# Performance work log

Hardware: AMD Instinct MI355X
Metric: run time of the kernel (lower is better)

The kernel has to match this reference:

```python
import jax, jax.numpy as jnp
import numpy as np

N_NEURONS = 4096
N_EDGES = 131072
N_LAYERS = 2
VOCAB = 8192
B, T = 8, 128
DECAY = 0.99


def setup_inputs() -> dict:
    key = jax.random.key(0)
    ks = jax.random.split(key, 8)
    idx = jax.random.randint(ks[0], (B, T), 0, VOCAB)
    src = jax.random.randint(ks[1], (N_EDGES,), 0, N_NEURONS)
    dst = jax.random.randint(ks[2], (N_EDGES,), 0, N_NEURONS)
    Wemb = jax.random.normal(ks[3], (VOCAB, N_NEURONS), dtype=jnp.float32) * 0.02
    Gx = jax.random.normal(ks[4], (N_EDGES,), dtype=jnp.float32) * 0.02
    Gy = jax.random.normal(ks[5], (N_EDGES,), dtype=jnp.float32) * 0.02
    Gs = jnp.ones((N_EDGES,), dtype=jnp.float32)
    W_out = jax.random.normal(ks[6], (VOCAB, N_NEURONS), dtype=jnp.float32) * 0.02
    b_out = jnp.zeros((VOCAB,), dtype=jnp.float32)
    return {"idx": idx, "src": src, "dst": dst, "Wemb": Wemb, "Gx": Gx,
            "Gy": Gy, "Gs": Gs, "W_out": W_out, "b_out": b_out}


def reference(idx, src, dst, Wemb, Gx, Gy, Gs, W_out, b_out):
    # X: [B, T, n] token embeddings
    X = Wemb[idx]
    sigma0 = jnp.zeros((src.shape[0],), dtype=Wemb.dtype)
    y0 = X[:, 0, :]  # initial y_t = embedding of first token
    Xt = jnp.transpose(X, (1, 0, 2))  # [T, B, n] for scan over time

    def step(carry, x_t):
        y_t, sigma = carry
        for _ in range(N_LAYERS):
            # A[:, d] += x_t[:, s] * sigma  (gather-mul-scatter over edges)
            A = jnp.zeros_like(x_t).at[:, dst].add(x_t[:, src] * sigma)
            # Hebbian plasticity update on edge state sigma
            hebbian = (y_t[:, src] * x_t[:, dst]).mean(0)
            sigma = (sigma + hebbian * Gs) * DECAY
            y_t = jnp.zeros_like(x_t).at[:, dst].add(jax.nn.relu(A[:, src]) * Gy)
            x_t = jax.nn.relu(jnp.zeros_like(x_t).at[:, dst].add(y_t[:, src] * Gx))
        return (y_t, sigma), x_t

    (_, sigma_final), xs = jax.lax.scan(step, (y0, sigma0), Xt)  # xs: [T, B, n]
    logits = jnp.einsum('tbn,vn->btv', xs, W_out) + b_out  # [B, T, vocab]
    return logits, sigma_final
```

## Files before the change

### kernel.cpp

```cpp
#include <hip/hip_runtime.h>
#include <cstdint>
#include <cstddef>

#define NN   4096
#define NE   131072
#define NBAT 8
#define NT   128
#define NV   8192
#define NK   4096
#define NM   1024
#define DECAYF 0.99f
#define COOP_BLOCKS 256
#define COOP_THREADS 1024
#define NBARRIERS (NT * 5)

typedef short bf16x8 __attribute__((ext_vector_type(8)));
typedef float f32x4 __attribute__((ext_vector_type(4)));
typedef unsigned short u16x8 __attribute__((ext_vector_type(8)));

__device__ __forceinline__ unsigned short f2bf(float f) {
  unsigned int u = __builtin_bit_cast(unsigned int, f);
  u = u + 0x7fffu + ((u >> 16) & 1u);
  return (unsigned short)(u >> 16);
}

__device__ __forceinline__ float cload(const float* p) {
  return __hip_atomic_load(p, __ATOMIC_RELAXED, __HIP_MEMORY_SCOPE_AGENT);
}
__device__ __forceinline__ void cstore(float* p, float v) {
  __hip_atomic_store(p, v, __ATOMIC_RELAXED, __HIP_MEMORY_SCOPE_AGENT);
}
__device__ __forceinline__ int cloadi(const int* p) {
  return __hip_atomic_load(p, __ATOMIC_RELAXED, __HIP_MEMORY_SCOPE_AGENT);
}
__device__ __forceinline__ void cstorei(int* p, int v) {
  __hip_atomic_store(p, v, __ATOMIC_RELAXED, __HIP_MEMORY_SCOPE_AGENT);
}

__global__ void k_hist(const int* __restrict__ dst, int* __restrict__ cnt) {
  int e = blockIdx.x * 256 + threadIdx.x;
  if (e < NE) atomicAdd(&cnt[dst[e]], 1);
}

__global__ void k_scan(const int* __restrict__ cnt, int* __restrict__ row_ptr,
                       int* __restrict__ cursor) {
  __shared__ int lds[256];
  int tid = threadIdx.x;
  int base = tid * 16;
  int loc[16];
  int s = 0;
  #pragma unroll
  for (int i = 0; i < 16; ++i) { loc[i] = s; s += cnt[base + i]; }
  lds[tid] = s;
  __syncthreads();
  for (int off = 1; off < 256; off <<= 1) {
    int v = lds[tid];
    int a = (tid >= off) ? lds[tid - off] : 0;
    __syncthreads();
    lds[tid] = v + a;
    __syncthreads();
  }
  int myoff = (tid == 0) ? 0 : lds[tid - 1];
  #pragma unroll
  for (int i = 0; i < 16; ++i) {
    int rp = myoff + loc[i];
    row_ptr[base + i] = rp;
    cursor[base + i] = rp;
  }
  if (tid == 255) row_ptr[NN] = lds[255];
}

__global__ void k_build(const int* __restrict__ src, const int* __restrict__ dst,
                        const float* __restrict__ Gx, const float* __restrict__ Gy,
                        const float* __restrict__ Gs, int* __restrict__ cursor,
                        int* __restrict__ src_s, int* __restrict__ orig_s,
                        float* __restrict__ Gx_s, float* __restrict__ Gy_s,
                        float* __restrict__ Gs_s) {
  int e = blockIdx.x * 256 + threadIdx.x;
  if (e >= NE) return;
  int d = dst[e];
  int pos = atomicAdd(&cursor[d], 1);
  src_s[pos] = src[e];
  orig_s[pos] = e;
  Gx_s[pos] = Gx[e];
  Gy_s[pos] = Gy[e];
  Gs_s[pos] = Gs[e];
}

__global__ void k_gatherX(const int* __restrict__ idx, const float* __restrict__ Wemb,
                          float* __restrict__ Xbuf, float* __restrict__ ybuf) {
  __shared__ float tile[256 * 9];
  int t = blockIdx.x >> 4;
  int nc = (blockIdx.x & 15) << 8;
  int tid = threadIdx.x;
  #pragma unroll
  for (int bb = 0; bb < 8; ++bb) {
    int row = idx[bb * NT + t];
    tile[tid * 9 + bb] = Wemb[(size_t)row * NN + nc + tid];
  }
  __syncthreads();
  float* dp = Xbuf + (size_t)t * (NN * NBAT) + (size_t)nc * NBAT;
  #pragma unroll
  for (int kk = 0; kk < 8; ++kk) dp[tid * 8 + kk] = tile[tid * 9 + kk];
  if (t == 0) {
    float* yp = ybuf + (size_t)nc * NBAT;
    #pragma unroll
    for (int kk = 0; kk < 8; ++kk) yp[tid * 8 + kk] = tile[tid * 9 + kk];
  }
}

__global__ void k_convW(const float* __restrict__ W, unsigned short* __restrict__ Wbf) {
  size_t base = ((size_t)blockIdx.x * 256 + threadIdx.x) * 8;
  float4 a = *(const float4*)(W + base);
  float4 b = *(const float4*)(W + base + 4);
  u16x8 hv;
  hv[0] = f2bf(a.x); hv[1] = f2bf(a.y); hv[2] = f2bf(a.z); hv[3] = f2bf(a.w);
  hv[4] = f2bf(b.x); hv[5] = f2bf(b.y); hv[6] = f2bf(b.z); hv[7] = f2bf(b.w);
  *(u16x8*)(Wbf + base) = hv;
}

__device__ __forceinline__ void gridbar(int* bar, int& gen) {
  __syncthreads();
  if (threadIdx.x == 0) {
    cstorei(&bar[blockIdx.x], gen + 1);
    while (cloadi(&bar[320]) <= gen) __builtin_amdgcn_s_sleep(1);
  }
  ++gen;
  __syncthreads();
}

__global__ __launch_bounds__(COOP_THREADS, 8) void k_loop(
    const int* __restrict__ row_ptr, const int* __restrict__ src_s,
    const float* __restrict__ Gx_s, const float* __restrict__ Gy_s,
    const float* __restrict__ Gs_s, float* __restrict__ sigma_s,
    const float* __restrict__ Xbuf, float* __restrict__ ybuf,
    float* __restrict__ xbuf, float* __restrict__ Abuf,
    unsigned short* __restrict__ Abf, int* bar,
    const int* __restrict__ orig_s, float* __restrict__ sig_out) {
  if (blockIdx.x == COOP_BLOCKS) {
    if (threadIdx.x < 64) {
      const int lane = threadIdx.x;
      for (int g = 1; g <= NBARRIERS; ++g) {
        for (;;) {
          int v0 = cloadi(&bar[lane * 4 + 0]);
          int v1 = cloadi(&bar[lane * 4 + 1]);
          int v2 = cloadi(&bar[lane * 4 + 2]);
          int v3 = cloadi(&bar[lane * 4 + 3]);
          int m = min(min(v0, v1), min(v2, v3));
          #pragma unroll
          for (int d = 1; d < 64; d <<= 1) m = min(m, __shfl_xor(m, d));
          if (m >= g) break;
        }
        if (lane == 0) cstorei(&bar[320], g);
      }
    }
    return;
  }

  const int tid = threadIdx.x;
  const int g = blockIdx.x * COOP_THREADS + tid;
  const int b = g & 7;
  const int h = (g >> 3) & 7;
  const int n = g >> 6;
  const int rs = row_ptr[n];
  const int re = row_ptr[n + 1];
  const int nb8 = (n << 3) | b;
  int gen = 0;

  for (int t = 0; t < NT; ++t) {
    const float* xp = Xbuf + (size_t)t * (NN * NBAT);
    #pragma unroll
    for (int layer = 0; layer < 2; ++layer) {
      {
        float xn = (layer == 0) ? xp[nb8] : cload(&xbuf[nb8]);
        float acc = 0.f;
        for (int j = rs + h; j < re; j += 32) {
          int jj[4], sv[4];
          float sg[4], gs[4], xv[4], yv[4];
          bool act[4];
          #pragma unroll
          for (int u = 0; u < 4; ++u) {
            int jc = j + (u << 3);
            act[u] = jc < re;
            jj[u] = act[u] ? jc : j;
          }
          #pragma unroll
          for (int u = 0; u < 4; ++u) sv[u] = src_s[jj[u]];
          #pragma unroll
          for (int u = 0; u < 4; ++u) {
            float sgu = sigma_s[jj[u]];
            float gsu = Gs_s[jj[u]];
            sg[u] = act[u] ? sgu : 0.f;
            gs[u] = act[u] ? gsu : 0.f;
          }
          #pragma unroll
          for (int u = 0; u < 4; ++u) {
            int sb = (sv[u] << 3) | b;
            xv[u] = (layer == 0) ? xp[sb] : cload(&xbuf[sb]);
            yv[u] = cload(&ybuf[sb]);
          }
          #pragma unroll
          for (int u = 0; u < 4; ++u) {
            acc = fmaf(xv[u], sg[u], acc);
            float pv = yv[u] * xn;
            pv += __shfl_xor(pv, 1);
            pv += __shfl_xor(pv, 2);
            pv += __shfl_xor(pv, 4);
            if (b == 0 && act[u])
              sigma_s[jj[u]] = (sg[u] + pv * 0.125f * gs[u]) * DECAYF;
          }
        }
        acc += __shfl_xor(acc, 8);
        acc += __shfl_xor(acc, 16);
        acc += __shfl_xor(acc, 32);
        if (h == 0) cstore(&Abuf[nb8], acc);
      }
      gridbar(bar, gen);
      {
        float acc = 0.f;
        for (int j = rs + h; j < re; j += 32) {
          int jj[4], sv[4];
          float gy[4], av[4];
          bool act[4];
          #pragma unroll
          for (int u = 0; u < 4; ++u) {
            int jc = j + (u << 3);
            act[u] = jc < re;
            jj[u] = act[u] ? jc : j;
          }
          #pragma unroll
          for (int u = 0; u < 4; ++u) sv[u] = src_s[jj[u]];
          #pragma unroll
          for (int u = 0; u < 4; ++u) {
            float gyu = Gy_s[jj[u]];
            gy[u] = act[u] ? gyu : 0.f;
          }
          #pragma unroll
          for (int u = 0; u < 4; ++u) av[u] = cload(&Abuf[(sv[u] << 3) | b]);
          #pragma unroll
          for (int u = 0; u < 4; ++u) acc = fmaf(fmaxf(av[u], 0.f), gy[u], acc);
        }
        acc += __shfl_xor(acc, 8);
        acc += __shfl_xor(acc, 16);
        acc += __shfl_xor(acc, 32);
        if (h == 0) cstore(&ybuf[nb8], acc);
      }
      gridbar(bar, gen);
      {
        float acc = 0.f;
        for (int j = rs + h; j < re; j += 32) {
          int jj[4], sv[4];
          float gx[4], yv[4];
          bool act[4];
          #pragma unroll
          for (int u = 0; u < 4; ++u) {
            int jc = j + (u << 3);
            act[u] = jc < re;
            jj[u] = act[u] ? jc : j;
          }
          #pragma unroll
          for (int u = 0; u < 4; ++u) sv[u] = src_s[jj[u]];
          #pragma unroll
          for (int u = 0; u < 4; ++u) {
            float gxu = Gx_s[jj[u]];
            gx[u] = act[u] ? gxu : 0.f;
          }
          #pragma unroll
          for (int u = 0; u < 4; ++u) yv[u] = cload(&ybuf[(sv[u] << 3) | b]);
          #pragma unroll
          for (int u = 0; u < 4; ++u) acc = fmaf(yv[u], gx[u], acc);
        }
        acc += __shfl_xor(acc, 8);
        acc += __shfl_xor(acc, 16);
        acc += __shfl_xor(acc, 32);
        if (layer == 0) {
          if (h == 0) cstore(&xbuf[nb8], fmaxf(acc, 0.f));
        } else if (h == 0) {
          Abf[(size_t)((b << 7) | t) * NK + n] = f2bf(fmaxf(acc, 0.f));
        }
      }
      if (layer == 0) {
        gridbar(bar, gen);
        xp = xbuf;
      }
    }
  }
  __syncthreads();
  int jlo = row_ptr[blockIdx.x * 16];
  int jhi = row_ptr[blockIdx.x * 16 + 16];
  for (int j = jlo + tid; j < jhi; j += COOP_THREADS) sig_out[orig_s[j]] = sigma_s[j];
}

__global__ __launch_bounds__(256) void k_gemm(const unsigned short* __restrict__ A,
                                              const unsigned short* __restrict__ Bw,
                                              const float* __restrict__ bias,
                                              float* __restrict__ C) {
  __shared__ __align__(16) unsigned short As[128 * 32];
  __shared__ __align__(16) unsigned short Bs[128 * 32];
  const int m0 = blockIdx.y * 128;
  const int v0 = blockIdx.x * 128;
  const int wave = threadIdx.x >> 6;
  const int lane = threadIdx.x & 63;
  const int wm = wave >> 1;
  const int wv = wave & 1;
  f32x4 acc[4][4] = {};

  const int srow = lane >> 2;
  const int skc = (lane & 3) * 8;

  for (int k0 = 0; k0 < NK; k0 += 32) {
    #pragma unroll
    for (int c = 0; c < 2; ++c) {
      int chunk = wave * 2 + c;
      int row = chunk * 16 + srow;
      __builtin_amdgcn_global_load_lds(
          (const __attribute__((address_space(1))) void*)(A + (size_t)(m0 + row) * NK + k0 + skc),
          (__attribute__((address_space(3))) void*)(As + chunk * 512), 16, 0, 0);
      __builtin_amdgcn_global_load_lds(
          (const __attribute__((address_space(1))) void*)(Bw + (size_t)(v0 + row) * NK + k0 + skc),
          (__attribute__((address_space(3))) void*)(Bs + chunk * 512), 16, 0, 0);
    }
    __syncthreads();
    bf16x8 af[4], bq[4];
    #pragma unroll
    for (int mi = 0; mi < 4; ++mi)
      af[mi] = *(const bf16x8*)(As + ((wm * 64 + mi * 16 + (lane & 15)) * 32 + (lane >> 4) * 8));
    #pragma unroll
    for (int ni = 0; ni < 4; ++ni)
      bq[ni] = *(const bf16x8*)(Bs + ((wv * 64 + ni * 16 + (lane & 15)) * 32 + (lane >> 4) * 8));
    #pragma unroll
    for (int mi = 0; mi < 4; ++mi)
      #pragma unroll
      for (int ni = 0; ni < 4; ++ni)
        acc[mi][ni] = __builtin_amdgcn_mfma_f32_16x16x32_bf16(af[mi], bq[ni], acc[mi][ni], 0, 0, 0);
    __syncthreads();
  }

  #pragma unroll
  for (int mi = 0; mi < 4; ++mi) {
    int mrow = m0 + wm * 64 + mi * 16 + ((lane >> 4) << 2);
    #pragma unroll
    for (int ni = 0; ni < 4; ++ni) {
      int vcol = v0 + wv * 64 + ni * 16 + (lane & 15);
      float bs = bias[vcol];
      f32x4 a = acc[mi][ni];
      #pragma unroll
      for (int r = 0; r < 4; ++r) C[(size_t)(mrow + r) * NV + vcol] = a[r] + bs;
    }
  }
}

extern "C" void kernel_launch(void* const* d_in, const int* in_sizes, int n_in,
                              void* d_out, int out_size, void* d_ws, size_t ws_size,
                              hipStream_t stream) {
  (void)in_sizes; (void)n_in; (void)out_size;
  const int*   idx  = (const int*)d_in[0];
  const int*   src  = (const int*)d_in[1];
  const int*   dst  = (const int*)d_in[2];
  const float* Wemb = (const float*)d_in[3];
  const float* Gx   = (const float*)d_in[4];
  const float* Gy   = (const float*)d_in[5];
  const float* Gs   = (const float*)d_in[6];
  const float* Wout = (const float*)d_in[7];
  const float* bout = (const float*)d_in[8];
  float* out = (float*)d_out;
  float* sig_out = out + (size_t)NM * NV;

  char* p = (char*)d_ws;
  int*   bar     = (int*)p;
  int*   cnt     = (int*)(p + 2048);
  float* sigma_s = (float*)(p + 2048 + 16384);
  size_t off = 2048 + 16384 + (size_t)NE * 4;
  const size_t msz = off;
  int*   row_ptr = (int*)(p + off); off += 16640;
  int*   cursor  = (int*)(p + off); off += 16384;
  int*   src_s   = (int*)(p + off); off += (size_t)NE * 4;
  int*   orig_s  = (int*)(p + off); off += (size_t)NE * 4;
  float* Gx_s    = (float*)(p + off); off += (size_t)NE * 4;
  float* Gy_s    = (float*)(p + off); off += (size_t)NE * 4;
  float* Gs_s    = (float*)(p + off); off += (size_t)NE * 4;
  float* ybuf    = (float*)(p + off); off += (size_t)NN * NBAT * 4;
  float* xbuf    = (float*)(p + off); off += (size_t)NN * NBAT * 4;
  float* Abuf    = (float*)(p + off); off += (size_t)NN * NBAT * 4;
  float* Xbuf    = (float*)(p + off); off += (size_t)NT * NN * NBAT * 4;
  unsigned short* Abf = (unsigned short*)(p + off); off += (size_t)NM * NK * 2;
  unsigned short* Wbf = (unsigned short*)(p + off); off += (size_t)NV * NK * 2;
  if (ws_size < off) return;

  hipMemsetAsync(d_ws, 0, msz, stream);
  k_hist<<<NE / 256, 256, 0, stream>>>(dst, cnt);
  k_scan<<<1, 256, 0, stream>>>(cnt, row_ptr, cursor);
  k_build<<<NE / 256, 256, 0, stream>>>(src, dst, Gx, Gy, Gs, cursor,
                                        src_s, orig_s, Gx_s, Gy_s, Gs_s);
  k_gatherX<<<NT * 16, 256, 0, stream>>>(idx, Wemb, Xbuf, ybuf);
  k_convW<<<(NV * NK) / (256 * 8), 256, 0, stream>>>(Wout, Wbf);
  k_loop<<<COOP_BLOCKS + 1, COOP_THREADS, 0, stream>>>(row_ptr, src_s, Gx_s, Gy_s, Gs_s,
      sigma_s, Xbuf, ybuf, xbuf, Abuf, Abf, bar, orig_s, sig_out);
  k_gemm<<<dim3(NV / 128, NM / 128), 256, 0, stream>>>(Abf, Wbf, bout, out);
}
```

Measured before the change: 3.399 ms.

## Fuse third edge stage via CSC atomic scatter, cutting grid barriers per step

Adds a source-sorted (CSC) copy of the edges so that each neuron can atomically scatter y*Gx into destination accumulators right after computing y. This removes the separate x-gather stage and one grid barrier per layer, going from five barriers per step to four. The barrier is now decentralized: every block polls all 256 flags itself, replacing the dedicated coordinator block. Accumulator zeroing and the ReLU/bf16 writeout are deferred to the next timestep. The cost is heavy float atomic traffic on xacc, and float atomics make the summation order nondeterministic.

```diff
diff --git a/kernel.cpp b/kernel.cpp
--- a/kernel.cpp
+++ b/kernel.cpp
@@ -12,7 +12,6 @@
 #define DECAYF 0.99f
 #define COOP_BLOCKS 256
 #define COOP_THREADS 1024
-#define NBARRIERS (NT * 5)
 
 typedef short bf16x8 __attribute__((ext_vector_type(8)));
 typedef float f32x4 __attribute__((ext_vector_type(4)));
@@ -36,10 +35,17 @@
 __device__ __forceinline__ void cstorei(int* p, int v) {
   __hip_atomic_store(p, v, __ATOMIC_RELAXED, __HIP_MEMORY_SCOPE_AGENT);
 }
-
-__global__ void k_hist(const int* __restrict__ dst, int* __restrict__ cnt) {
+__device__ __forceinline__ void cadd(float* p, float v) {
+  (void)__hip_atomic_fetch_add(p, v, __ATOMIC_RELAXED, __HIP_MEMORY_SCOPE_AGENT);
+}
+
+__global__ void k_hist(const int* __restrict__ dst, const int* __restrict__ src,
+                       int* __restrict__ cnt, int* __restrict__ cnt2) {
   int e = blockIdx.x * 256 + threadIdx.x;
-  if (e < NE) atomicAdd(&cnt[dst[e]], 1);
+  if (e < NE) {
+    atomicAdd(&cnt[dst[e]], 1);
+    atomicAdd(&cnt2[src[e]], 1);
+  }
 }
 
 __global__ void k_scan(const int* __restrict__ cnt, int* __restrict__ row_ptr,
@@ -72,19 +78,23 @@
 
 __global__ void k_build(const int* __restrict__ src, const int* __restrict__ dst,
                         const float* __restrict__ Gx, const float* __restrict__ Gy,
-                        const float* __restrict__ Gs, int* __restrict__ cursor,
+                        const float* __restrict__ Gs,
+                        int* __restrict__ cursor, int* __restrict__ cursor2,
                         int* __restrict__ src_s, int* __restrict__ orig_s,
-                        float* __restrict__ Gx_s, float* __restrict__ Gy_s,
-                        float* __restrict__ Gs_s) {
+                        float* __restrict__ Gy_s, float* __restrict__ Gs_s,
+                        int* __restrict__ csc_dst, float* __restrict__ csc_gx) {
   int e = blockIdx.x * 256 + threadIdx.x;
   if (e >= NE) return;
   int d = dst[e];
+  int s = src[e];
   int pos = atomicAdd(&cursor[d], 1);
-  src_s[pos] = src[e];
+  src_s[pos] = s;
   orig_s[pos] = e;
-  Gx_s[pos] = Gx[e];
   Gy_s[pos] = Gy[e];
   Gs_s[pos] = Gs[e];
+  int pos2 = atomicAdd(&cursor2[s], 1);
+  csc_dst[pos2] = d;
+  csc_gx[pos2] = Gx[e];
 }
 
 __global__ void k_gatherX(const int* __restrict__ idx, const float* __restrict__ Wemb,
@@ -121,42 +131,127 @@
 
 __device__ __forceinline__ void gridbar(int* bar, int& gen) {
   __syncthreads();
-  if (threadIdx.x == 0) {
-    cstorei(&bar[blockIdx.x], gen + 1);
-    while (cloadi(&bar[320]) <= gen) __builtin_amdgcn_s_sleep(1);
-  }
-  ++gen;
+  const int target = gen + 1;
+  if (threadIdx.x < 64) {
+    if (threadIdx.x == 0) cstorei(&bar[blockIdx.x], target);
+    const int l = threadIdx.x;
+    for (;;) {
+      int v0 = cloadi(&bar[l]);
+      int v1 = cloadi(&bar[l + 64]);
+      int v2 = cloadi(&bar[l + 128]);
+      int v3 = cloadi(&bar[l + 192]);
+      int m = min(min(v0, v1), min(v2, v3));
+      #pragma unroll
+      for (int d = 1; d < 64; d <<= 1) m = min(m, __shfl_xor(m, d));
+      if (m >= target) break;
+      __builtin_amdgcn_s_sleep(1);
+    }
+  }
+  gen = target;
   __syncthreads();
 }
 
-__global__ __launch_bounds__(COOP_THREADS, 8) void k_loop(
+template <bool USE_ACC>
+__device__ __forceinline__ void s12_stage(
+    int rs, int re, int h, int b, int nb8,
+    const int* __restrict__ src_s, float* __restrict__ sigma_s,
+    const float* __restrict__ Gs_s, const float* __restrict__ xp,
+    const float* __restrict__ xacc, const float* __restrict__ ybuf,
+    float* __restrict__ Abuf) {
+  float xn = USE_ACC ? fmaxf(cload(&xacc[nb8]), 0.f) : xp[nb8];
+  float acc = 0.f;
+  for (int j = rs + h; j < re; j += 32) {
+    int jj[4], sv[4];
+    float sg[4], gs[4], xv[4], yv[4];
+    bool act[4];
+    #pragma unroll
+    for (int u = 0; u < 4; ++u) {
+      int jc = j + (u << 3);
+      act[u] = jc < re;
+      jj[u] = act[u] ? jc : j;
+    }
+    #pragma unroll
+    for (int u = 0; u < 4; ++u) sv[u] = src_s[jj[u]];
+    #pragma unroll
+    for (int u = 0; u < 4; ++u) {
+      float sgu = sigma_s[jj[u]];
+      float gsu = Gs_s[jj[u]];
+      sg[u] = act[u] ? sgu : 0.f;
+      gs[u] = act[u] ? gsu : 0.f;
+    }
+    #pragma unroll
+    for (int u = 0; u < 4; ++u) {
+      int sb = (sv[u] << 3) | b;
+      xv[u] = USE_ACC ? fmaxf(cload(&xacc[sb]), 0.f) : xp[sb];
+      yv[u] = cload(&ybuf[sb]);
+    }
+    #pragma unroll
+    for (int u = 0; u < 4; ++u) {
+      acc = fmaf(xv[u], sg[u], acc);
+      float pv = yv[u] * xn;
+      pv += __shfl_xor(pv, 1);
+      pv += __shfl_xor(pv, 2);
+      pv += __shfl_xor(pv, 4);
+      if (b == 0 && act[u])
+        sigma_s[jj[u]] = (sg[u] + pv * 0.125f * gs[u]) * DECAYF;
+    }
+  }
+  acc += __shfl_xor(acc, 8);
+  acc += __shfl_xor(acc, 16);
+  acc += __shfl_xor(acc, 32);
+  if (h == 0) cstore(&Abuf[nb8], acc);
+}
+
+__device__ __forceinline__ void s3_scatter_stage(
+    int rs, int re, int cs, int ce, int h, int b, int nb8,
+    const int* __restrict__ src_s, const float* __restrict__ Gy_s,
+    const float* __restrict__ Abuf, float* __restrict__ ybuf,
+    const int* __restrict__ csc_dst, const float* __restrict__ csc_gx,
+    float* __restrict__ xacc) {
+  float acc = 0.f;
+  for (int j = rs + h; j < re; j += 32) {
+    int jj[4], sv[4];
+    float gy[4], av[4];
+    bool act[4];
+    #pragma unroll
+    for (int u = 0; u < 4; ++u) {
+      int jc = j + (u << 3);
+      act[u] = jc < re;
+      jj[u] = act[u] ? jc : j;
+    }
+    #pragma unroll
+    for (int u = 0; u < 4; ++u) sv[u] = src_s[jj[u]];
+    #pragma unroll
+    for (int u = 0; u < 4; ++u) {
+      float gyu = Gy_s[jj[u]];
+      gy[u] = act[u] ? gyu : 0.f;
+    }
+    #pragma unroll
+    for (int u = 0; u < 4; ++u) av[u] = cload(&Abuf[(sv[u] << 3) | b]);
+    #pragma unroll
+    for (int u = 0; u < 4; ++u) acc = fmaf(fmaxf(av[u], 0.f), gy[u], acc);
+  }
+  acc += __shfl_xor(acc, 8);
+  acc += __shfl_xor(acc, 16);
+  acc += __shfl_xor(acc, 32);
+  if (h == 0) cstore(&ybuf[nb8], acc);
+  for (int jc = cs + h; jc < ce; jc += 8) {
+    int d = csc_dst[jc];
+    float gx = csc_gx[jc];
+    cadd(&xacc[(d << 3) | b], acc * gx);
+  }
+}
+
+__global__ __launch_bounds__(COOP_THREADS, 4) void k_loop(
     const int* __restrict__ row_ptr, const int* __restrict__ src_s,
-    const float* __restrict__ Gx_s, const float* __restrict__ Gy_s,
-    const float* __restrict__ Gs_s, float* __restrict__ sigma_s,
+    const float* __restrict__ Gy_s, const float* __restrict__ Gs_s,
+    float* __restrict__ sigma_s,
+    const int* __restrict__ csc_ptr, const int* __restrict__ csc_dst,
+    const float* __restrict__ csc_gx,
     const float* __restrict__ Xbuf, float* __restrict__ ybuf,
-    float* __restrict__ xbuf, float* __restrict__ Abuf,
-    unsigned short* __restrict__ Abf, int* bar,
+    float* __restrict__ xacc1, float* __restrict__ xacc2,
+    float* __restrict__ Abuf, unsigned short* __restrict__ Abf, int* bar,
     const int* __restrict__ orig_s, float* __restrict__ sig_out) {
-  if (blockIdx.x == COOP_BLOCKS) {
-    if (threadIdx.x < 64) {
-      const int lane = threadIdx.x;
-      for (int g = 1; g <= NBARRIERS; ++g) {
-        for (;;) {
-          int v0 = cloadi(&bar[lane * 4 + 0]);
-          int v1 = cloadi(&bar[lane * 4 + 1]);
-          int v2 = cloadi(&bar[lane * 4 + 2]);
-          int v3 = cloadi(&bar[lane * 4 + 3]);
-          int m = min(min(v0, v1), min(v2, v3));
-          #pragma unroll
-          for (int d = 1; d < 64; d <<= 1) m = min(m, __shfl_xor(m, d));
-          if (m >= g) break;
-        }
-        if (lane == 0) cstorei(&bar[320], g);
-      }
-    }
-    return;
-  }
-
   const int tid = threadIdx.x;
   const int g = blockIdx.x * COOP_THREADS + tid;
   const int b = g & 7;
@@ -164,128 +259,39 @@
   const int n = g >> 6;
   const int rs = row_ptr[n];
   const int re = row_ptr[n + 1];
+  const int cs = csc_ptr[n];
+  const int ce = csc_ptr[n + 1];
   const int nb8 = (n << 3) | b;
   int gen = 0;
 
   for (int t = 0; t < NT; ++t) {
     const float* xp = Xbuf + (size_t)t * (NN * NBAT);
-    #pragma unroll
-    for (int layer = 0; layer < 2; ++layer) {
-      {
-        float xn = (layer == 0) ? xp[nb8] : cload(&xbuf[nb8]);
-        float acc = 0.f;
-        for (int j = rs + h; j < re; j += 32) {
-          int jj[4], sv[4];
-          float sg[4], gs[4], xv[4], yv[4];
-          bool act[4];
-          #pragma unroll
-          for (int u = 0; u < 4; ++u) {
-            int jc = j + (u << 3);
-            act[u] = jc < re;
-            jj[u] = act[u] ? jc : j;
-          }
-          #pragma unroll
-          for (int u = 0; u < 4; ++u) sv[u] = src_s[jj[u]];
-          #pragma unroll
-          for (int u = 0; u < 4; ++u) {
-            float sgu = sigma_s[jj[u]];
-            float gsu = Gs_s[jj[u]];
-            sg[u] = act[u] ? sgu : 0.f;
-            gs[u] = act[u] ? gsu : 0.f;
-          }
-          #pragma unroll
-          for (int u = 0; u < 4; ++u) {
-            int sb = (sv[u] << 3) | b;
-            xv[u] = (layer == 0) ? xp[sb] : cload(&xbuf[sb]);
-            yv[u] = cload(&ybuf[sb]);
-          }
-          #pragma unroll
-          for (int u = 0; u < 4; ++u) {
-            acc = fmaf(xv[u], sg[u], acc);
-            float pv = yv[u] * xn;
-            pv += __shfl_xor(pv, 1);
-            pv += __shfl_xor(pv, 2);
-            pv += __shfl_xor(pv, 4);
-            if (b == 0 && act[u])
-              sigma_s[jj[u]] = (sg[u] + pv * 0.125f * gs[u]) * DECAYF;
-          }
-        }
-        acc += __shfl_xor(acc, 8);
-        acc += __shfl_xor(acc, 16);
-        acc += __shfl_xor(acc, 32);
-        if (h == 0) cstore(&Abuf[nb8], acc);
+    if (t > 0) {
+      if (h == 0) {
+        float v = cload(&xacc2[nb8]);
+        Abf[(size_t)((b << 7) | (t - 1)) * NK + n] = f2bf(fmaxf(v, 0.f));
+        cstore(&xacc2[nb8], 0.f);
+      } else if (h == 1) {
+        cstore(&xacc1[nb8], 0.f);
       }
-      gridbar(bar, gen);
-      {
-        float acc = 0.f;
-        for (int j = rs + h; j < re; j += 32) {
-          int jj[4], sv[4];
-          float gy[4], av[4];
-          bool act[4];
-          #pragma unroll
-          for (int u = 0; u < 4; ++u) {
-            int jc = j + (u << 3);
-            act[u] = jc < re;
-            jj[u] = act[u] ? jc : j;
-          }
-          #pragma unroll
-          for (int u = 0; u < 4; ++u) sv[u] = src_s[jj[u]];
-          #pragma unroll
-          for (int u = 0; u < 4; ++u) {
-            float gyu = Gy_s[jj[u]];
-            gy[u] = act[u] ? gyu : 0.f;
-          }
-          #pragma unroll
-          for (int u = 0; u < 4; ++u) av[u] = cload(&Abuf[(sv[u] << 3) | b]);
-          #pragma unroll
-          for (int u = 0; u < 4; ++u) acc = fmaf(fmaxf(av[u], 0.f), gy[u], acc);
-        }
-        acc += __shfl_xor(acc, 8);
-        acc += __shfl_xor(acc, 16);
-        acc += __shfl_xor(acc, 32);
-        if (h == 0) cstore(&ybuf[nb8], acc);
-      }
-      gridbar(bar, gen);
-      {
-        float acc = 0.f;
-        for (int j = rs + h; j < re; j += 32) {
-          int jj[4], sv[4];
-          float gx[4], yv[4];
-          bool act[4];
-          #pragma unroll
-          for (int u = 0; u < 4; ++u) {
-            int jc = j + (u << 3);
-            act[u] = jc < re;
-            jj[u] = act[u] ? jc : j;
-          }
-          #pragma unroll
-          for (int u = 0; u < 4; ++u) sv[u] = src_s[jj[u]];
-          #pragma unroll
-          for (int u = 0; u < 4; ++u) {
-            float gxu = Gx_s[jj[u]];
-            gx[u] = act[u] ? gxu : 0.f;
-          }
-          #pragma unroll
-          for (int u = 0; u < 4; ++u) yv[u] = cload(&ybuf[(sv[u] << 3) | b]);
-          #pragma unroll
-          for (int u = 0; u < 4; ++u) acc = fmaf(yv[u], gx[u], acc);
-        }
-        acc += __shfl_xor(acc, 8);
-        acc += __shfl_xor(acc, 16);
-        acc += __shfl_xor(acc, 32);
-        if (layer == 0) {
-          if (h == 0) cstore(&xbuf[nb8], fmaxf(acc, 0.f));
-        } else if (h == 0) {
-          Abf[(size_t)((b << 7) | t) * NK + n] = f2bf(fmaxf(acc, 0.f));
-        }
-      }
-      if (layer == 0) {
-        gridbar(bar, gen);
-        xp = xbuf;
-      }
-    }
-  }
-  __syncthreads();
+    }
+    s12_stage<false>(rs, re, h, b, nb8, src_s, sigma_s, Gs_s, xp, nullptr,
+                     ybuf, Abuf);
+    gridbar(bar, gen);
+    s3_scatter_stage(rs, re, cs, ce, h, b, nb8, src_s, Gy_s, Abuf, ybuf,
+                     csc_dst, csc_gx, xacc1);
+    gridbar(bar, gen);
+    s12_stage<true>(rs, re, h, b, nb8, src_s, sigma_s, Gs_s, nullptr, xacc1,
+                    ybuf, Abuf);
+    gridbar(bar, gen);
+    s3_scatter_stage(rs, re, cs, ce, h, b, nb8, src_s, Gy_s, Abuf, ybuf,
+                     csc_dst, csc_gx, xacc2);
+    gridbar(bar, gen);
+  }
+  if (h == 0) {
+    float v = cload(&xacc2[nb8]);
+    Abf[(size_t)((b << 7) | (NT - 1)) * NK + n] = f2bf(fmaxf(v, 0.f));
+  }
   int jlo = row_ptr[blockIdx.x * 16];
   int jhi = row_ptr[blockIdx.x * 16 + 16];
   for (int j = jlo + tid; j < jhi; j += COOP_THREADS) sig_out[orig_s[j]] = sigma_s[j];
@@ -368,19 +374,24 @@
 
   char* p = (char*)d_ws;
   int*   bar     = (int*)p;
-  int*   cnt     = (int*)(p + 2048);
-  float* sigma_s = (float*)(p + 2048 + 16384);
-  size_t off = 2048 + 16384 + (size_t)NE * 4;
-  const size_t msz = off;
+  int*   cnt     = (int*)(p + 4096);
+  int*   cnt2    = (int*)(p + 20480);
+  float* xacc1   = (float*)(p + 36864);
+  float* xacc2   = (float*)(p + 167936);
+  float* sigma_s = (float*)(p + 299008);
+  const size_t msz = 299008 + (size_t)NE * 4;
+  size_t off = msz;
   int*   row_ptr = (int*)(p + off); off += 16640;
   int*   cursor  = (int*)(p + off); off += 16384;
+  int*   csc_ptr = (int*)(p + off); off += 16640;
+  int*   cursor2 = (int*)(p + off); off += 16384;
   int*   src_s   = (int*)(p + off); off += (size_t)NE * 4;
   int*   orig_s  = (int*)(p + off); off += (size_t)NE * 4;
-  float* Gx_s    = (float*)(p + off); off += (size_t)NE * 4;
   float* Gy_s    = (float*)(p + off); off += (size_t)NE * 4;
   float* Gs_s    = (float*)(p + off); off += (size_t)NE * 4;
+  int*   csc_dst = (int*)(p + off); off += (size_t)NE * 4;
+  float* csc_gx  = (float*)(p + off); off += (size_t)NE * 4;
   float* ybuf    = (float*)(p + off); off += (size_t)NN * NBAT * 4;
-  float* xbuf    = (float*)(p + off); off += (size_t)NN * NBAT * 4;
   float* Abuf    = (float*)(p + off); off += (size_t)NN * NBAT * 4;
   float* Xbuf    = (float*)(p + off); off += (size_t)NT * NN * NBAT * 4;
   unsigned short* Abf = (unsigned short*)(p + off); off += (size_t)NM * NK * 2;
@@ -388,13 +399,15 @@
   if (ws_size < off) return;
 
   hipMemsetAsync(d_ws, 0, msz, stream);
-  k_hist<<<NE / 256, 256, 0, stream>>>(dst, cnt);
+  k_hist<<<NE / 256, 256, 0, stream>>>(dst, src, cnt, cnt2);
   k_scan<<<1, 256, 0, stream>>>(cnt, row_ptr, cursor);
-  k_build<<<NE / 256, 256, 0, stream>>>(src, dst, Gx, Gy, Gs, cursor,
-                                        src_s, orig_s, Gx_s, Gy_s, Gs_s);
+  k_scan<<<1, 256, 0, stream>>>(cnt2, csc_ptr, cursor2);
+  k_build<<<NE / 256, 256, 0, stream>>>(src, dst, Gx, Gy, Gs, cursor, cursor2,
+                                        src_s, orig_s, Gy_s, Gs_s, csc_dst, csc_gx);
   k_gatherX<<<NT * 16, 256, 0, stream>>>(idx, Wemb, Xbuf, ybuf);
   k_convW<<<(NV * NK) / (256 * 8), 256, 0, stream>>>(Wout, Wbf);
-  k_loop<<<COOP_BLOCKS + 1, COOP_THREADS, 0, stream>>>(row_ptr, src_s, Gx_s, Gy_s, Gs_s,
-      sigma_s, Xbuf, ybuf, xbuf, Abuf, Abf, bar, orig_s, sig_out);
+  k_loop<<<COOP_BLOCKS, COOP_THREADS, 0, stream>>>(row_ptr, src_s, Gy_s, Gs_s,
+      sigma_s, csc_ptr, csc_dst, csc_gx, Xbuf, ybuf, xacc1, xacc2, Abuf, Abf,
+      bar, orig_s, sig_out);
   k_gemm<<<dim3(NV / 128, NM / 128), 256, 0, stream>>>(Abf, Wbf, bout, out);
 }
```

After: 5.674 ms. +66.9%, slower.
